# Optimization experiments

Hardware: AMD Instinct MI355X
Metric: run time of the kernel (lower is better)

Reference implementation:

```python
import jax, jax.numpy as jnp
import numpy as np

N_IMG, C_IN, H, W = 8, 8, 136, 200
N_INST = 512
CHANNELS = 8
STRIDE = 8
MASK_OUT_STRIDE = 4
# sizes_of_interest + [last*2], per __init__
SOI = jnp.asarray([64.0, 128.0, 256.0, 512.0, 1024.0, 2048.0], dtype=jnp.float32)
W_NUMS = [(C_IN + 2) * CHANNELS, CHANNELS * CHANNELS, CHANNELS]
B_NUMS = [CHANNELS, CHANNELS, 1]
N_PARAMS = sum(W_NUMS) + sum(B_NUMS)  # 169


def compute_locations(h, w, stride):
    # matches adet compute_locations: centers of stride-sized cells, (x, y)
    shifts_x = jnp.arange(w, dtype=jnp.float32) * stride + stride // 2
    shifts_y = jnp.arange(h, dtype=jnp.float32) * stride + stride // 2
    ys, xs = jnp.meshgrid(shifts_y, shifts_x, indexing='ij')
    return jnp.stack([xs.reshape(-1), ys.reshape(-1)], axis=1)  # [h*w, 2]


def bilinear_up_align_corners(x, out_h, out_w):
    # x: [n, h, w]; F.interpolate(mode='bilinear', align_corners=True)
    n, h, w = x.shape
    ys = jnp.linspace(0.0, h - 1.0, out_h)
    xs = jnp.linspace(0.0, w - 1.0, out_w)
    y0 = jnp.floor(ys).astype(jnp.int32)
    x0 = jnp.floor(xs).astype(jnp.int32)
    y1 = jnp.minimum(y0 + 1, h - 1)
    x1 = jnp.minimum(x0 + 1, w - 1)
    wy = (ys - y0.astype(jnp.float32))[None, :, None]
    wx = (xs - x0.astype(jnp.float32))[None, None, :]
    top = x[:, y0, :]
    bot = x[:, y1, :]
    row0 = top[:, :, x0] * (1.0 - wx) + top[:, :, x1] * wx
    row1 = bot[:, :, x0] * (1.0 - wx) + bot[:, :, x1] * wx
    return row0 * (1.0 - wy) + row1 * wy


def dice_coefficient(x, target):
    eps = 1e-5
    n = x.shape[0]
    x = x.reshape(n, -1)
    target = target.reshape(n, -1)
    intersection = jnp.sum(x * target, axis=1)
    union = jnp.sum(x * x, axis=1) + jnp.sum(target * target, axis=1) + eps
    return 1.0 - 2.0 * intersection / union


def setup_inputs() -> dict:
    key = jax.random.key(0)
    ks = jax.random.split(key, 6)
    mask_feats = jax.random.normal(ks[0], (N_IMG, C_IN, H, W), jnp.float32)
    mask_head_params = jax.random.normal(ks[1], (N_INST, N_PARAMS), jnp.float32) * 0.1
    instance_locations = jax.random.uniform(ks[2], (N_INST, 2), jnp.float32) * jnp.asarray(
        [W * STRIDE, H * STRIDE], dtype=jnp.float32)
    gt_masks = (jax.random.uniform(ks[3], (N_INST, 2 * H, 2 * W), jnp.float32) > 0.5).astype(jnp.float32)
    im_inds = jax.random.randint(ks[4], (N_INST,), 0, N_IMG, jnp.int32)
    fpn_levels = jax.random.randint(ks[5], (N_INST,), 0, 5, jnp.int32)
    return {
        'mask_feats': mask_feats,
        'mask_head_params': mask_head_params,
        'instance_locations': instance_locations,
        'gt_masks': gt_masks,
        'im_inds': im_inds,
        'fpn_levels': fpn_levels,
        'mask_feat_stride': 8,
    }


def reference(mask_feats, mask_head_params, instance_locations, gt_masks, im_inds, fpn_levels, mask_feat_stride):
    n_inst = mask_head_params.shape[0]
    # relative coordinates: instance center minus every grid location, / size-of-interest
    locations = compute_locations(H, W, mask_feat_stride)          # [H*W, 2]
    rel = instance_locations[:, None, :] - locations[None, :, :]   # [n, H*W, 2]
    rel = jnp.transpose(rel, (0, 2, 1)) / SOI[fpn_levels][:, None, None]
    rel = rel.reshape(n_inst, 2, H, W)
    feats = mask_feats[im_inds]                                    # gather [n, C_IN, H, W]
    x = jnp.concatenate([rel, feats], axis=1)                      # [n, C_IN+2, H, W]

    # parse_dynamic_params: split per-instance params into 1x1 conv weights/biases
    splits = np.cumsum(W_NUMS + B_NUMS)[:-1].tolist()
    p = jnp.split(mask_head_params, splits, axis=1)
    w0 = p[0].reshape(n_inst, CHANNELS, C_IN + 2)
    w1 = p[1].reshape(n_inst, CHANNELS, CHANNELS)
    w2 = p[2].reshape(n_inst, 1, CHANNELS)
    b0, b1, b2 = p[3], p[4], p[5]

    # grouped 1x1 convs (groups = n_inst) == per-instance channel GEMM
    x = jax.nn.relu(jnp.einsum('nchw,noc->nohw', x, w0) + b0[:, :, None, None])
    x = jax.nn.relu(jnp.einsum('nchw,noc->nohw', x, w1) + b1[:, :, None, None])
    logits = jnp.einsum('nchw,noc->nohw', x, w2) + b2[:, :, None, None]  # [n, 1, H, W]

    up = mask_feat_stride // MASK_OUT_STRIDE
    logits_up = bilinear_up_align_corners(logits[:, 0], H * up, W * up)
    scores = jax.nn.sigmoid(logits_up)
    loss = dice_coefficient(scores, gt_masks)                      # [n]
    return loss
```

## Files before the change

kernel.cpp:

```cpp
#include <hip/hip_runtime.h>
#include <math.h>

#define NIMG 8
#define CIN 8
#define Hh 136
#define Ww 200
#define HW (Hh * Ww)
#define OH 272
#define OW 400
#define NINST 512
#define NPAR 169
#define TROWS 34
#define NTILES 8
#define LROWS 19
#define IT_PX 512
#define QSTRIDE 36
#define HBUF_WORDS (128 * QSTRIDE)

#define PIN(x) asm volatile("" : "+v"(x))

__global__ __launch_bounds__(256, 2) void dmh_fused2(
    const float* __restrict__ feats,
    const float* __restrict__ pars,
    const float* __restrict__ iloc,
    const float* __restrict__ gt,
    const int* __restrict__ iminds,
    const int* __restrict__ lvls,
    float* __restrict__ part)
{
    __shared__ float hbuf[HBUF_WORDS];
    __shared__ float slog[LROWS * Ww];
    __shared__ float sred[12];

    const int n    = blockIdx.y;
    const int tile = blockIdx.x;
    const int tid  = threadIdx.x;
    const int qi   = tid & 127;
    const int half = tid >> 7;

    const float ix = iloc[2 * n + 0];
    const float iy = iloc[2 * n + 1];
    const int   im = iminds[n];
    const float invsoi = 1.0f / (float)(64 << lvls[n]);

    const float* pp = pars + n * NPAR;

    float Wf[32], A0[4], Ax[4], Ay[4];
#pragma unroll
    for (int j = 0; j < 4; j++) {
        const int o = half * 4 + j;
        const float wx0 = pp[o * 10 + 0];
        const float wy0 = pp[o * 10 + 1];
        Ax[j] = -8.0f * invsoi * wx0;
        Ay[j] = -8.0f * invsoi * wy0;
        A0[j] = pp[152 + o] + (wx0 * (ix - 4.0f) + wy0 * (iy - 4.0f)) * invsoi;
#pragma unroll
        for (int c = 0; c < 8; c++) Wf[j * 8 + c] = pp[o * 10 + 2 + c];
    }
    float w1[64], w2[8], b1[8], b2;
#pragma unroll
    for (int i = 0; i < 64; i++) w1[i] = pp[80 + i];
#pragma unroll
    for (int i = 0; i < 8; i++)  w2[i] = pp[144 + i];
#pragma unroll
    for (int i = 0; i < 8; i++)  b1[i] = pp[160 + i];
    b2 = pp[168];

#pragma unroll
    for (int i = 0; i < 32; i++) PIN(Wf[i]);
#pragma unroll
    for (int i = 0; i < 4; i++) { PIN(A0[i]); PIN(Ax[i]); PIN(Ay[i]); }
#pragma unroll
    for (int i = 0; i < 64; i++) PIN(w1[i]);
#pragma unroll
    for (int i = 0; i < 8; i++) { PIN(w2[i]); PIN(b1[i]); }
    PIN(b2);

    const float sy = 135.0f / 271.0f;
    const float sx = 199.0f / 399.0f;

    const int oy0 = tile * TROWS;
    const int ly0 = (int)((float)oy0 * sy);
    int lyL = (int)((float)(oy0 + TROWS - 1) * sy) + 1;
    if (lyL > Hh - 1) lyL = Hh - 1;
    const int lycnt = lyL - ly0 + 1;
    const int npix  = lycnt * Ww;

    const float* fb0 = feats + (size_t)im * (CIN * HW) + ly0 * Ww;

    const int niter = (npix + IT_PX - 1) / IT_PX;
    for (int it = 0; it < niter; it++) {
        const int base = it * IT_PX;
        const int cnt  = (npix - base < IT_PX) ? (npix - base) : IT_PX;

        if (qi * 4 < cnt) {
            const int lpx = base + qi * 4;
            const int yy  = lpx / Ww;
            const int x   = lpx - yy * Ww;
            const float yf = (float)(ly0 + yy);
            const float* fb = fb0 + lpx;
            float f[8][4];
#pragma unroll
            for (int c = 0; c < 8; c++) {
                const float4 t = *reinterpret_cast<const float4*>(fb + c * HW);
                f[c][0] = t.x; f[c][1] = t.y; f[c][2] = t.z; f[c][3] = t.w;
            }
            float* hb = &hbuf[qi * QSTRIDE + half * 4];
#pragma unroll
            for (int p = 0; p < 4; p++) {
                const float xf = (float)(x + p);
                float4 hv;
                float* hvp = (float*)&hv;
#pragma unroll
                for (int j = 0; j < 4; j++) {
                    float a = A0[j] + Ax[j] * xf + Ay[j] * yf;
#pragma unroll
                    for (int c = 0; c < 8; c++) a += Wf[j * 8 + c] * f[c][p];
                    hvp[j] = fmaxf(a, 0.0f);
                }
                *reinterpret_cast<float4*>(hb + p * 8) = hv;
            }
        }
        __syncthreads();

#pragma unroll
        for (int s = 0; s < 2; s++) {
            const int pl = tid + s * 256;
            if (pl < cnt) {
                const int q = pl >> 2, p = pl & 3;
                const float* hb = &hbuf[q * QSTRIDE + p * 8];
                const float4 h0 = *reinterpret_cast<const float4*>(hb);
                const float4 h1 = *reinterpret_cast<const float4*>(hb + 4);
                const float hv[8] = { h0.x, h0.y, h0.z, h0.w, h1.x, h1.y, h1.z, h1.w };
                float lg = b2;
#pragma unroll
                for (int o = 0; o < 8; o++) {
                    float a = b1[o];
#pragma unroll
                    for (int c = 0; c < 8; c++) a += w1[o * 8 + c] * hv[c];
                    lg += w2[o] * fmaxf(a, 0.0f);
                }
                slog[base + pl] = lg;
            }
        }
        __syncthreads();
    }

    float aI = 0.0f, aS = 0.0f, aT = 0.0f;
    const float* gtn = gt + (size_t)n * (OH * OW) + (size_t)oy0 * OW;
    for (int g4 = tid; g4 < TROWS * (OW / 4); g4 += 256) {
        const int ry = g4 / 100;
        const int gx = (g4 - ry * 100) * 4;
        const int oy = oy0 + ry;
        const float ysf = (float)oy * sy;
        const int y0 = (int)ysf;
        const float wy = ysf - (float)y0;
        const int y1 = (y0 + 1 > Hh - 1) ? (Hh - 1) : (y0 + 1);
        int r0i = y0 - ly0, r1i = y1 - ly0;
        r0i = r0i < 0 ? 0 : (r0i > lycnt - 1 ? lycnt - 1 : r0i);
        r1i = r1i < 0 ? 0 : (r1i > lycnt - 1 ? lycnt - 1 : r1i);
        const float* s0 = &slog[r0i * Ww];
        const float* s1 = &slog[r1i * Ww];

        const float4 t4 = *reinterpret_cast<const float4*>(gtn + ry * OW + gx);
        const float tv[4] = { t4.x, t4.y, t4.z, t4.w };
#pragma unroll
        for (int p = 0; p < 4; p++) {
            const int ox = gx + p;
            const float xsf = (float)ox * sx;
            const int x0 = (int)xsf;
            const float wx = xsf - (float)x0;
            const int x1 = (x0 + 1 > Ww - 1) ? (Ww - 1) : (x0 + 1);
            const float v00 = s0[x0];
            const float v01 = s0[x1];
            const float v10 = s1[x0];
            const float v11 = s1[x1];
            const float top = v00 + wx * (v01 - v00);
            const float bot = v10 + wx * (v11 - v10);
            const float v   = top + wy * (bot - top);
            const float sg  = __fdividef(1.0f, 1.0f + __expf(-v));
            aI += sg * tv[p];
            aS += sg * sg;
            aT += tv[p];
        }
    }

#pragma unroll
    for (int off = 32; off > 0; off >>= 1) {
        aI += __shfl_down(aI, off, 64);
        aS += __shfl_down(aS, off, 64);
        aT += __shfl_down(aT, off, 64);
    }
    const int wv = tid >> 6;
    if ((tid & 63) == 0) {
        sred[wv * 3 + 0] = aI;
        sred[wv * 3 + 1] = aS;
        sred[wv * 3 + 2] = aT;
    }
    __syncthreads();
    if (tid == 0) {
        float* pt = part + (size_t)(n * NTILES + tile) * 3;
        pt[0] = sred[0] + sred[3] + sred[6] + sred[9];
        pt[1] = sred[1] + sred[4] + sred[7] + sred[10];
        pt[2] = sred[2] + sred[5] + sred[8] + sred[11];
    }
}

__global__ __launch_bounds__(256) void dmh_fin2(const float* __restrict__ part,
                                                float* __restrict__ out)
{
    const int i = blockIdx.x * 256 + threadIdx.x;
    if (i < NINST) {
        float I = 0.0f, S = 0.0f, T = 0.0f;
#pragma unroll
        for (int t = 0; t < NTILES; t++) {
            const float* pt = part + (size_t)(i * NTILES + t) * 3;
            I += pt[0]; S += pt[1]; T += pt[2];
        }
        out[i] = 1.0f - 2.0f * I / (S + T + 1e-5f);
    }
}

extern "C" void kernel_launch(void* const* d_in, const int* in_sizes, int n_in,
                              void* d_out, int out_size, void* d_ws, size_t ws_size,
                              hipStream_t stream) {
    const float* feats  = (const float*)d_in[0];
    const float* pars   = (const float*)d_in[1];
    const float* iloc   = (const float*)d_in[2];
    const float* gt     = (const float*)d_in[3];
    const int*   iminds = (const int*)d_in[4];
    const int*   lvls   = (const int*)d_in[5];

    float* part = (float*)d_ws;
    dim3 grid(NTILES, NINST);
    dmh_fused2<<<grid, 256, 0, stream>>>(feats, pars, iloc, gt, iminds, lvls, part);
    dmh_fin2<<<(NINST + 255) / 256, 256, 0, stream>>>(part, (float*)d_out);
}
```

Before: 453.1 us.

## Stage per-instance weights in LDS and compute full MLP per thread

Per-instance conv weights move out of pinned registers into a small shared-memory table that a few threads fill once. Each thread now runs both 1x1 conv layers for four pixels, which removes the hidden-activation LDS buffer and the two barriers per iteration. Launch bounds go from two to four blocks per SM to raise occupancy. The cost is a broadcast LDS read for every weight use, plus more live registers per thread (32 hidden values), which may spill under the tighter register budget.

```diff
diff --git a/kernel.cpp b/kernel.cpp
--- a/kernel.cpp
+++ b/kernel.cpp
@@ -13,13 +13,15 @@
 #define TROWS 34
 #define NTILES 8
 #define LROWS 19
-#define IT_PX 512
-#define QSTRIDE 36
-#define HBUF_WORDS (128 * QSTRIDE)
-
-#define PIN(x) asm volatile("" : "+v"(x))
-
-__global__ __launch_bounds__(256, 2) void dmh_fused2(
+
+#define WOFF_WF 0
+#define WOFF_AC 64
+#define WOFF_W1 96
+#define WOFF_B1 160
+#define WOFF_W2 168
+#define WOFF_B2 176
+
+__global__ __launch_bounds__(256, 4) void dmh_fused3(
     const float* __restrict__ feats,
     const float* __restrict__ pars,
     const float* __restrict__ iloc,
@@ -28,53 +30,42 @@
     const int* __restrict__ lvls,
     float* __restrict__ part)
 {
-    __shared__ float hbuf[HBUF_WORDS];
-    __shared__ float slog[LROWS * Ww];
+    __shared__ __align__(16) float swt[192];
+    __shared__ __align__(16) float slog[LROWS * Ww];
     __shared__ float sred[12];
 
     const int n    = blockIdx.y;
     const int tile = blockIdx.x;
     const int tid  = threadIdx.x;
-    const int qi   = tid & 127;
-    const int half = tid >> 7;
-
-    const float ix = iloc[2 * n + 0];
-    const float iy = iloc[2 * n + 1];
+
     const int   im = iminds[n];
-    const float invsoi = 1.0f / (float)(64 << lvls[n]);
-
     const float* pp = pars + n * NPAR;
 
-    float Wf[32], A0[4], Ax[4], Ay[4];
-#pragma unroll
-    for (int j = 0; j < 4; j++) {
-        const int o = half * 4 + j;
+    if (tid < 8) {
+        const int o = tid;
+        const float ix = iloc[2 * n + 0];
+        const float iy = iloc[2 * n + 1];
+        const float invsoi = 1.0f / (float)(64 << lvls[n]);
         const float wx0 = pp[o * 10 + 0];
         const float wy0 = pp[o * 10 + 1];
-        Ax[j] = -8.0f * invsoi * wx0;
-        Ay[j] = -8.0f * invsoi * wy0;
-        A0[j] = pp[152 + o] + (wx0 * (ix - 4.0f) + wy0 * (iy - 4.0f)) * invsoi;
-#pragma unroll
-        for (int c = 0; c < 8; c++) Wf[j * 8 + c] = pp[o * 10 + 2 + c];
-    }
-    float w1[64], w2[8], b1[8], b2;
-#pragma unroll
-    for (int i = 0; i < 64; i++) w1[i] = pp[80 + i];
-#pragma unroll
-    for (int i = 0; i < 8; i++)  w2[i] = pp[144 + i];
-#pragma unroll
-    for (int i = 0; i < 8; i++)  b1[i] = pp[160 + i];
-    b2 = pp[168];
-
-#pragma unroll
-    for (int i = 0; i < 32; i++) PIN(Wf[i]);
-#pragma unroll
-    for (int i = 0; i < 4; i++) { PIN(A0[i]); PIN(Ax[i]); PIN(Ay[i]); }
-#pragma unroll
-    for (int i = 0; i < 64; i++) PIN(w1[i]);
-#pragma unroll
-    for (int i = 0; i < 8; i++) { PIN(w2[i]); PIN(b1[i]); }
-    PIN(b2);
+        swt[WOFF_AC + o * 4 + 0] = pp[152 + o] + (wx0 * (ix - 4.0f) + wy0 * (iy - 4.0f)) * invsoi;
+        swt[WOFF_AC + o * 4 + 1] = -8.0f * invsoi * wx0;
+        swt[WOFF_AC + o * 4 + 2] = -8.0f * invsoi * wy0;
+        swt[WOFF_AC + o * 4 + 3] = 0.0f;
+#pragma unroll
+        for (int c = 0; c < 8; c++) swt[WOFF_WF + o * 8 + c] = pp[o * 10 + 2 + c];
+    } else if (tid < 16) {
+        const int o = tid - 8;
+#pragma unroll
+        for (int c = 0; c < 8; c++) swt[WOFF_W1 + o * 8 + c] = pp[80 + o * 8 + c];
+    } else if (tid == 16) {
+#pragma unroll
+        for (int o = 0; o < 8; o++) swt[WOFF_B1 + o] = pp[160 + o];
+    } else if (tid == 17) {
+#pragma unroll
+        for (int o = 0; o < 8; o++) swt[WOFF_W2 + o] = pp[144 + o];
+        swt[WOFF_B2] = pp[168];
+    }
 
     const float sy = 135.0f / 271.0f;
     const float sx = 199.0f / 399.0f;
@@ -84,67 +75,64 @@
     int lyL = (int)((float)(oy0 + TROWS - 1) * sy) + 1;
     if (lyL > Hh - 1) lyL = Hh - 1;
     const int lycnt = lyL - ly0 + 1;
-    const int npix  = lycnt * Ww;
+    const int nq    = lycnt * (Ww / 4);
 
     const float* fb0 = feats + (size_t)im * (CIN * HW) + ly0 * Ww;
 
-    const int niter = (npix + IT_PX - 1) / IT_PX;
-    for (int it = 0; it < niter; it++) {
-        const int base = it * IT_PX;
-        const int cnt  = (npix - base < IT_PX) ? (npix - base) : IT_PX;
-
-        if (qi * 4 < cnt) {
-            const int lpx = base + qi * 4;
-            const int yy  = lpx / Ww;
-            const int x   = lpx - yy * Ww;
-            const float yf = (float)(ly0 + yy);
-            const float* fb = fb0 + lpx;
-            float f[8][4];
-#pragma unroll
-            for (int c = 0; c < 8; c++) {
-                const float4 t = *reinterpret_cast<const float4*>(fb + c * HW);
-                f[c][0] = t.x; f[c][1] = t.y; f[c][2] = t.z; f[c][3] = t.w;
+    __syncthreads();
+
+    for (int q = tid; q < nq; q += 256) {
+        const int yy = q / 50;
+        const int xq = (q - yy * 50) * 4;
+        const float yf = (float)(ly0 + yy);
+        const float* fb = fb0 + yy * Ww + xq;
+        float f[8][4];
+#pragma unroll
+        for (int c = 0; c < 8; c++) {
+            const float4 t = *reinterpret_cast<const float4*>(fb + c * HW);
+            f[c][0] = t.x; f[c][1] = t.y; f[c][2] = t.z; f[c][3] = t.w;
+        }
+
+        float h[8][4];
+#pragma unroll
+        for (int o = 0; o < 8; o++) {
+            const float4 wA  = *reinterpret_cast<const float4*>(&swt[WOFF_AC + o * 4]);
+            const float4 wf0 = *reinterpret_cast<const float4*>(&swt[WOFF_WF + o * 8]);
+            const float4 wf1 = *reinterpret_cast<const float4*>(&swt[WOFF_WF + o * 8 + 4]);
+            const float py = wA.x + wA.z * yf;
+#pragma unroll
+            for (int p = 0; p < 4; p++) {
+                float a = py + wA.y * (float)(xq + p);
+                a += wf0.x * f[0][p]; a += wf0.y * f[1][p];
+                a += wf0.z * f[2][p]; a += wf0.w * f[3][p];
+                a += wf1.x * f[4][p]; a += wf1.y * f[5][p];
+                a += wf1.z * f[6][p]; a += wf1.w * f[7][p];
+                h[o][p] = fmaxf(a, 0.0f);
             }
-            float* hb = &hbuf[qi * QSTRIDE + half * 4];
+        }
+
+        const float b2v = swt[WOFF_B2];
+        float lg[4] = { b2v, b2v, b2v, b2v };
+#pragma unroll
+        for (int o = 0; o < 8; o++) {
+            const float4 w10 = *reinterpret_cast<const float4*>(&swt[WOFF_W1 + o * 8]);
+            const float4 w11 = *reinterpret_cast<const float4*>(&swt[WOFF_W1 + o * 8 + 4]);
+            const float b1o = swt[WOFF_B1 + o];
+            const float w2o = swt[WOFF_W2 + o];
 #pragma unroll
             for (int p = 0; p < 4; p++) {
-                const float xf = (float)(x + p);
-                float4 hv;
-                float* hvp = (float*)&hv;
-#pragma unroll
-                for (int j = 0; j < 4; j++) {
-                    float a = A0[j] + Ax[j] * xf + Ay[j] * yf;
-#pragma unroll
-                    for (int c = 0; c < 8; c++) a += Wf[j * 8 + c] * f[c][p];
-                    hvp[j] = fmaxf(a, 0.0f);
-                }
-                *reinterpret_cast<float4*>(hb + p * 8) = hv;
+                float a = b1o;
+                a += w10.x * h[0][p]; a += w10.y * h[1][p];
+                a += w10.z * h[2][p]; a += w10.w * h[3][p];
+                a += w11.x * h[4][p]; a += w11.y * h[5][p];
+                a += w11.z * h[6][p]; a += w11.w * h[7][p];
+                lg[p] += w2o * fmaxf(a, 0.0f);
             }
         }
-        __syncthreads();
-
-#pragma unroll
-        for (int s = 0; s < 2; s++) {
-            const int pl = tid + s * 256;
-            if (pl < cnt) {
-                const int q = pl >> 2, p = pl & 3;
-                const float* hb = &hbuf[q * QSTRIDE + p * 8];
-                const float4 h0 = *reinterpret_cast<const float4*>(hb);
-                const float4 h1 = *reinterpret_cast<const float4*>(hb + 4);
-                const float hv[8] = { h0.x, h0.y, h0.z, h0.w, h1.x, h1.y, h1.z, h1.w };
-                float lg = b2;
-#pragma unroll
-                for (int o = 0; o < 8; o++) {
-                    float a = b1[o];
-#pragma unroll
-                    for (int c = 0; c < 8; c++) a += w1[o * 8 + c] * hv[c];
-                    lg += w2[o] * fmaxf(a, 0.0f);
-                }
-                slog[base + pl] = lg;
-            }
-        }
-        __syncthreads();
-    }
+        *reinterpret_cast<float4*>(&slog[q * 4]) =
+            make_float4(lg[0], lg[1], lg[2], lg[3]);
+    }
+    __syncthreads();
 
     float aI = 0.0f, aS = 0.0f, aT = 0.0f;
     const float* gtn = gt + (size_t)n * (OH * OW) + (size_t)oy0 * OW;
@@ -233,6 +221,6 @@
 
     float* part = (float*)d_ws;
     dim3 grid(NTILES, NINST);
-    dmh_fused2<<<grid, 256, 0, stream>>>(feats, pars, iloc, gt, iminds, lvls, part);
+    dmh_fused3<<<grid, 256, 0, stream>>>(feats, pars, iloc, gt, iminds, lvls, part);
     dmh_fin2<<<(NINST + 255) / 256, 256, 0, stream>>>(part, (float*)d_out);
 }
```

New measurement: 1.686 ms. +272.2%, slower.
